# Optimization experiments

Hardware: AMD Instinct MI355X
Metric: run time of the kernel (lower is better)

The kernel has to match this reference:

```python
import jax, jax.numpy as jnp
import numpy as np

N = 400000  # active sparse points (voxels)
K = 27      # 3^3 kernel offsets (dimension=3, kernel_size=3)
C = 32      # inplanes == planes
EPS = 1e-5


def sparse_conv(x, nbr, mask, W, b):
    # gather-GEMM-scatter: for each kernel offset k, out += x[nbr[:,k]] @ W[k]
    # missing neighbors are masked out (MinkowskiEngine skips absent pairs).
    xg = x[nbr] * mask[..., None].astype(x.dtype)   # [N, K, C]
    return jnp.einsum('nkc,kcd->nd', xg, W) + b     # [N, C]


def batchnorm(h, gamma, beta):
    # MinkowskiBatchNorm: per-channel stats over all active points
    mean = jnp.mean(h, axis=0)
    var = jnp.mean(jnp.square(h - mean), axis=0)
    return (h - mean) * jax.lax.rsqrt(var + EPS) * gamma + beta


def setup_inputs() -> dict:
    key = jax.random.key(0)
    ks = jax.random.split(key, 13)
    x = jax.random.normal(ks[0], (N, C), dtype=jnp.float32)
    nbr1 = jax.random.randint(ks[1], (N, K), 0, N, dtype=jnp.int32)
    mask1 = jax.random.randint(ks[2], (N, K), 0, 2, dtype=jnp.int32).astype(bool)
    nbr2 = jax.random.randint(ks[3], (N, K), 0, N, dtype=jnp.int32)
    mask2 = jax.random.randint(ks[4], (N, K), 0, 2, dtype=jnp.int32).astype(bool)
    s = 1.0 / np.sqrt(K * C)  # kaiming-ish scale for sparse conv kernels
    W1 = jax.random.normal(ks[5], (K, C, C), dtype=jnp.float32) * s
    b1 = jax.random.normal(ks[6], (C,), dtype=jnp.float32) * 0.01
    W2 = jax.random.normal(ks[7], (K, C, C), dtype=jnp.float32) * s
    b2 = jax.random.normal(ks[8], (C,), dtype=jnp.float32) * 0.01
    gamma1 = jnp.ones((C,), jnp.float32)
    beta1 = jnp.zeros((C,), jnp.float32)
    gamma2 = jnp.ones((C,), jnp.float32)
    beta2 = jnp.zeros((C,), jnp.float32)
    return dict(x=x, W1=W1, b1=b1, gamma1=gamma1, beta1=beta1,
                W2=W2, b2=b2, gamma2=gamma2, beta2=beta2,
                nbr1=nbr1, mask1=mask1, nbr2=nbr2, mask2=mask2)


def reference(x, W1, b1, gamma1, beta1, W2, b2, gamma2, beta2,
              nbr1, mask1, nbr2, mask2):
    residual = x  # downsample = Identity (stride=1)
    out = sparse_conv(x, nbr1, mask1, W1, b1)
    out = jax.nn.relu(batchnorm(out, gamma1, beta1))
    out = sparse_conv(out, nbr2, mask2, W2, b2)
    out = batchnorm(out, gamma2, beta2)
    out = out + residual  # drop_path=0.0 -> Identity
    return jax.nn.relu(out)
```

## Files before the change

### kernel.cpp

```cpp
#include <hip/hip_runtime.h>

#define NPTS 400000
#define KK 27
#define CC 32
#define EPSV 1e-5f
#define LSTRIDE 29

using bf8_t = __attribute__((ext_vector_type(8))) __bf16;
using f4_t  = __attribute__((ext_vector_type(4))) float;
using us8_t = __attribute__((ext_vector_type(8))) unsigned short;

__device__ __forceinline__ unsigned short f2bf(float f) {
    unsigned int u = __float_as_uint(f);
    u += 0x7FFF + ((u >> 16) & 1u);
    return (unsigned short)(u >> 16);
}

#define WBLOCKS 216
__global__ __launch_bounds__(256) void cvt_all(
    const float* __restrict__ x,
    const float* __restrict__ W1, const float* __restrict__ W2,
    unsigned short* __restrict__ xb,
    unsigned short* __restrict__ Wt1, unsigned short* __restrict__ Wt2,
    float* __restrict__ sums)
{
    const int bid = blockIdx.x;
    if (bid < WBLOCKS) {
        if (bid == 0) sums[threadIdx.x] = 0.f;
        const int id = bid * 256 + threadIdx.x;
        const int which = id >= KK * CC * CC;
        const int t = which ? id - KK * CC * CC : id;
        const int k = t >> 10, d = (t >> 5) & 31, c = t & 31;
        const float* W = which ? W2 : W1;
        unsigned short* Wt = which ? Wt2 : Wt1;
        Wt[t] = f2bf(W[k * 1024 + c * CC + d]);
        return;
    }
    const size_t base = ((size_t)(bid - WBLOCKS) * 256 + threadIdx.x) * 8;
    if (base >= (size_t)NPTS * CC) return;
    const f4_t v0 = __builtin_nontemporal_load((const f4_t*)(x + base));
    const f4_t v1 = __builtin_nontemporal_load((const f4_t*)(x + base + 4));
    us8_t o;
#pragma unroll
    for (int j = 0; j < 8; ++j) o[j] = f2bf(j < 4 ? v0[j] : v1[j - 4]);
    *(us8_t*)(xb + base) = o;
}

__global__ __launch_bounds__(512, 6) void conv_mfma(
    const unsigned short* __restrict__ xb,
    const unsigned short* __restrict__ Wt,
    const float* __restrict__ bias,
    const int* __restrict__ nbr,
    const int* __restrict__ mask,
    float* __restrict__ out,
    float* __restrict__ sums)
{
    __shared__ int lidx[128 * LSTRIDE];
    __shared__ float rs[8][CC], rq[8][CC];

    const int t = threadIdx.x;
    const int P0 = blockIdx.x * 128;

    const int* nb = nbr + (size_t)P0 * KK;
    const int* mb = mask + (size_t)P0 * KK;
    for (int i = t; i < 128 * KK; i += 512) {
        const int p = i / KK;
        const int k = i - p * KK;
        const int nv = __builtin_nontemporal_load(nb + i);
        const int mv = __builtin_nontemporal_load(mb + i);
        lidx[p * LSTRIDE + k] = mv ? nv : -1;
    }
    __syncthreads();

    const int wave = t >> 6;
    const int lane = t & 63;
    const int m = lane & 15;
    const int q = lane >> 4;
    const int p0 = P0 + wave * 16;

    const int* rowA = lidx + (wave * 16 + m) * LSTRIDE;

    f4_t acc00 = {}, acc01 = {};

#pragma unroll
    for (int kb = 0; kb < 3; ++kb) {
        int idx[9];
#pragma unroll
        for (int j = 0; j < 9; ++j) idx[j] = rowA[kb * 9 + j];
        bf8_t A0[9];
#pragma unroll
        for (int j = 0; j < 9; ++j) {
            bf8_t t0 = {};
            if (idx[j] >= 0) t0 = *(const bf8_t*)(xb + (size_t)idx[j] * CC + q * 8);
            A0[j] = t0;
        }
#pragma unroll
        for (int j = 0; j < 9; ++j) {
            const unsigned short* wk = Wt + (kb * 9 + j) * (CC * CC) + q * 8;
            const bf8_t w0 = *(const bf8_t*)(wk + m * CC);
            const bf8_t w1 = *(const bf8_t*)(wk + (m + 16) * CC);
            acc00 = __builtin_amdgcn_mfma_f32_16x16x32_bf16(A0[j], w0, acc00, 0, 0, 0);
            acc01 = __builtin_amdgcn_mfma_f32_16x16x32_bf16(A0[j], w1, acc01, 0, 0, 0);
        }
    }

    const float b0 = bias[m], b1 = bias[m + 16];
    float s0 = 0.f, q0 = 0.f, s1 = 0.f, q1 = 0.f;
    const int prow = p0 + q * 4;
#pragma unroll
    for (int r = 0; r < 4; ++r) {
        const float v0 = acc00[r] + b0;
        const float v1 = acc01[r] + b1;
        __builtin_nontemporal_store(v0, out + (size_t)(prow + r) * CC + m);
        __builtin_nontemporal_store(v1, out + (size_t)(prow + r) * CC + m + 16);
        s0 += v0; q0 += v0 * v0;
        s1 += v1; q1 += v1 * v1;
    }
    s0 += __shfl_down(s0, 32, 64); s0 += __shfl_down(s0, 16, 64);
    q0 += __shfl_down(q0, 32, 64); q0 += __shfl_down(q0, 16, 64);
    s1 += __shfl_down(s1, 32, 64); s1 += __shfl_down(s1, 16, 64);
    q1 += __shfl_down(q1, 32, 64); q1 += __shfl_down(q1, 16, 64);

    if (lane < 16) {
        rs[wave][m] = s0;      rq[wave][m] = q0;
        rs[wave][m + 16] = s1; rq[wave][m + 16] = q1;
    }
    __syncthreads();
    if (t < CC) {
        float ssum = 0.f, qsum = 0.f;
#pragma unroll
        for (int w = 0; w < 8; ++w) { ssum += rs[w][t]; qsum += rq[w][t]; }
        atomicAdd(&sums[t], ssum);
        atomicAdd(&sums[CC + t], qsum);
    }
}

__global__ __launch_bounds__(256) void bn_relu_bf16(
    const float* __restrict__ h, const float* __restrict__ sums,
    const float* __restrict__ gamma, const float* __restrict__ beta,
    unsigned short* __restrict__ buf)
{
    const size_t base = ((size_t)blockIdx.x * 256 + threadIdx.x) * 8;
    if (base >= (size_t)NPTS * CC) return;
    const int d0 = (int)(base & (CC - 1));
    const f4_t v0 = __builtin_nontemporal_load((const f4_t*)(h + base));
    const f4_t v1 = __builtin_nontemporal_load((const f4_t*)(h + base + 4));
    us8_t o;
#pragma unroll
    for (int j = 0; j < 8; ++j) {
        const int d = d0 + j;
        const float mean = sums[d] * (1.f / NPTS);
        const float var = sums[CC + d] * (1.f / NPTS) - mean * mean;
        const float sc = gamma[d] * rsqrtf(var + EPSV);
        const float x = (j < 4 ? v0[j] : v1[j - 4]);
        o[j] = f2bf(fmaxf((x - mean) * sc + beta[d], 0.f));
    }
    *(us8_t*)(buf + base) = o;
}

__global__ __launch_bounds__(256) void bn_res_relu_kernel(
    float* __restrict__ out, const float* __restrict__ sums,
    const float* __restrict__ gamma, const float* __restrict__ beta,
    const float* __restrict__ x)
{
    const size_t i = (size_t)blockIdx.x * 256 + threadIdx.x;
    const size_t base = i * 4;
    if (base >= (size_t)NPTS * CC) return;
    const int d0 = (int)(base & (CC - 1));
    const f4_t v  = __builtin_nontemporal_load((const f4_t*)(out + base));
    const f4_t rx = __builtin_nontemporal_load((const f4_t*)(x + base));
    f4_t r;
#pragma unroll
    for (int j = 0; j < 4; ++j) {
        const int d = d0 + j;
        const float mean = sums[d] * (1.f / NPTS);
        const float var = sums[CC + d] * (1.f / NPTS) - mean * mean;
        const float sc = gamma[d] * rsqrtf(var + EPSV);
        r[j] = fmaxf((v[j] - mean) * sc + beta[d] + rx[j], 0.f);
    }
    __builtin_nontemporal_store(r, (f4_t*)(out + base));
}

extern "C" void kernel_launch(void* const* d_in, const int* in_sizes, int n_in,
                              void* d_out, int out_size, void* d_ws, size_t ws_size,
                              hipStream_t stream) {
    const float* x   = (const float*)d_in[0];
    const float* W1  = (const float*)d_in[1];
    const float* b1  = (const float*)d_in[2];
    const float* g1  = (const float*)d_in[3];
    const float* be1 = (const float*)d_in[4];
    const float* W2  = (const float*)d_in[5];
    const float* b2  = (const float*)d_in[6];
    const float* g2  = (const float*)d_in[7];
    const float* be2 = (const float*)d_in[8];
    const int* nbr1  = (const int*)d_in[9];
    const int* mask1 = (const int*)d_in[10];
    const int* nbr2  = (const int*)d_in[11];
    const int* mask2 = (const int*)d_in[12];

    float* out = (float*)d_out;

    float* sums          = (float*)d_ws;
    unsigned short* xbuf = (unsigned short*)((char*)d_ws + 1024);
    unsigned short* Wt1  = xbuf + (size_t)NPTS * CC;
    unsigned short* Wt2  = Wt1 + KK * CC * CC;

    const int cvt_blocks = WBLOCKS + (NPTS * CC / 8 + 255) / 256;

    cvt_all<<<cvt_blocks, 256, 0, stream>>>(x, W1, W2, xbuf, Wt1, Wt2, sums);
    conv_mfma<<<NPTS / 128, 512, 0, stream>>>(xbuf, Wt1, b1, nbr1, mask1, out, sums);
    bn_relu_bf16<<<(NPTS * CC / 8 + 255) / 256, 256, 0, stream>>>(out, sums, g1, be1, xbuf);
    conv_mfma<<<NPTS / 128, 512, 0, stream>>>(xbuf, Wt2, b2, nbr2, mask2, out, sums + 64);
    bn_res_relu_kernel<<<(NPTS * CC / 4 + 255) / 256, 256, 0, stream>>>(out, sums + 64, g2, be2, x);
}
```

Before: 511.9 us.

## Fuse BN1+ReLU into conv2 gather and store conv outputs as bf16

Removes the standalone BN1+ReLU pass: conv1 now writes bf16 pre-activations into the output buffer, and conv2 applies the per-channel scale/shift and ReLU to each gathered neighbor row before the MFMA. Conv2 also writes bf16 output into the xbuf region, which the final BN+residual+ReLU kernel reads. This removes one full elementwise pass and halves intermediate traffic. In exchange, BN1 math is redone on every gathered row (27 times per point), and the pre-BN values are rounded to bf16 before normalization.

After: 530.2 us. 1.04x slower.

```diff
diff --git a/kernel.cpp b/kernel.cpp
--- a/kernel.cpp
+++ b/kernel.cpp
@@ -14,6 +14,9 @@
     unsigned int u = __float_as_uint(f);
     u += 0x7FFF + ((u >> 16) & 1u);
     return (unsigned short)(u >> 16);
+}
+__device__ __forceinline__ float bf2f(unsigned short s) {
+    return __uint_as_float((unsigned)s << 16);
 }
 
 #define WBLOCKS 216
@@ -46,13 +49,13 @@
     *(us8_t*)(xb + base) = o;
 }
 
-__global__ __launch_bounds__(512, 6) void conv_mfma(
+__global__ __launch_bounds__(512, 6) void conv1_mfma(
     const unsigned short* __restrict__ xb,
     const unsigned short* __restrict__ Wt,
     const float* __restrict__ bias,
     const int* __restrict__ nbr,
     const int* __restrict__ mask,
-    float* __restrict__ out,
+    unsigned short* __restrict__ hb,
     float* __restrict__ sums)
 {
     __shared__ int lidx[128 * LSTRIDE];
@@ -111,8 +114,8 @@
     for (int r = 0; r < 4; ++r) {
         const float v0 = acc00[r] + b0;
         const float v1 = acc01[r] + b1;
-        __builtin_nontemporal_store(v0, out + (size_t)(prow + r) * CC + m);
-        __builtin_nontemporal_store(v1, out + (size_t)(prow + r) * CC + m + 16);
+        __builtin_nontemporal_store(f2bf(v0), hb + (size_t)(prow + r) * CC + m);
+        __builtin_nontemporal_store(f2bf(v1), hb + (size_t)(prow + r) * CC + m + 16);
         s0 += v0; q0 += v0 * v0;
         s1 += v1; q1 += v1 * v1;
     }
@@ -135,50 +138,145 @@
     }
 }
 
-__global__ __launch_bounds__(256) void bn_relu_bf16(
-    const float* __restrict__ h, const float* __restrict__ sums,
+__global__ __launch_bounds__(512, 6) void conv2_mfma(
+    const unsigned short* __restrict__ hb,
+    const unsigned short* __restrict__ Wt,
+    const float* __restrict__ bias,
+    const float* __restrict__ g1, const float* __restrict__ be1,
+    const float* __restrict__ sums1,
+    const int* __restrict__ nbr,
+    const int* __restrict__ mask,
+    unsigned short* __restrict__ h2b,
+    float* __restrict__ sums)
+{
+    __shared__ int lidx[128 * LSTRIDE];
+    __shared__ float rs[8][CC], rq[8][CC];
+
+    const int t = threadIdx.x;
+    const int P0 = blockIdx.x * 128;
+
+    const int* nb = nbr + (size_t)P0 * KK;
+    const int* mb = mask + (size_t)P0 * KK;
+    for (int i = t; i < 128 * KK; i += 512) {
+        const int p = i / KK;
+        const int k = i - p * KK;
+        const int nv = __builtin_nontemporal_load(nb + i);
+        const int mv = __builtin_nontemporal_load(mb + i);
+        lidx[p * LSTRIDE + k] = mv ? nv : -1;
+    }
+    __syncthreads();
+
+    const int wave = t >> 6;
+    const int lane = t & 63;
+    const int m = lane & 15;
+    const int q = lane >> 4;
+    const int p0 = P0 + wave * 16;
+
+    float sc_[8], sh_[8];
+#pragma unroll
+    for (int e = 0; e < 8; ++e) {
+        const int c = q * 8 + e;
+        const float mean = sums1[c] * (1.f / NPTS);
+        const float var = sums1[CC + c] * (1.f / NPTS) - mean * mean;
+        const float s = g1[c] * rsqrtf(var + EPSV);
+        sc_[e] = s;
+        sh_[e] = be1[c] - mean * s;
+    }
+
+    const int* rowA = lidx + (wave * 16 + m) * LSTRIDE;
+
+    f4_t acc00 = {}, acc01 = {};
+
+#pragma unroll
+    for (int kb = 0; kb < 3; ++kb) {
+        int idx[9];
+#pragma unroll
+        for (int j = 0; j < 9; ++j) idx[j] = rowA[kb * 9 + j];
+        bf8_t A0[9];
+#pragma unroll
+        for (int j = 0; j < 9; ++j) {
+            bf8_t a = {};
+            if (idx[j] >= 0) {
+                const us8_t raw = *(const us8_t*)(hb + (size_t)idx[j] * CC + q * 8);
+                us8_t o;
+#pragma unroll
+                for (int e = 0; e < 8; ++e)
+                    o[e] = f2bf(fmaxf(bf2f(raw[e]) * sc_[e] + sh_[e], 0.f));
+                a = __builtin_bit_cast(bf8_t, o);
+            }
+            A0[j] = a;
+        }
+#pragma unroll
+        for (int j = 0; j < 9; ++j) {
+            const unsigned short* wk = Wt + (kb * 9 + j) * (CC * CC) + q * 8;
+            const bf8_t w0 = *(const bf8_t*)(wk + m * CC);
+            const bf8_t w1 = *(const bf8_t*)(wk + (m + 16) * CC);
+            acc00 = __builtin_amdgcn_mfma_f32_16x16x32_bf16(A0[j], w0, acc00, 0, 0, 0);
+            acc01 = __builtin_amdgcn_mfma_f32_16x16x32_bf16(A0[j], w1, acc01, 0, 0, 0);
+        }
+    }
+
+    const float b0 = bias[m], b1 = bias[m + 16];
+    float s0 = 0.f, q0 = 0.f, s1 = 0.f, q1 = 0.f;
+    const int prow = p0 + q * 4;
+#pragma unroll
+    for (int r = 0; r < 4; ++r) {
+        const float v0 = acc00[r] + b0;
+        const float v1 = acc01[r] + b1;
+        __builtin_nontemporal_store(f2bf(v0), h2b + (size_t)(prow + r) * CC + m);
+        __builtin_nontemporal_store(f2bf(v1), h2b + (size_t)(prow + r) * CC + m + 16);
+        s0 += v0; q0 += v0 * v0;
+        s1 += v1; q1 += v1 * v1;
+    }
+    s0 += __shfl_down(s0, 32, 64); s0 += __shfl_down(s0, 16, 64);
+    q0 += __shfl_down(q0, 32, 64); q0 += __shfl_down(q0, 16, 64);
+    s1 += __shfl_down(s1, 32, 64); s1 += __shfl_down(s1, 16, 64);
+    q1 += __shfl_down(q1, 32, 64); q1 += __shfl_down(q1, 16, 64);
+
+    if (lane < 16) {
+        rs[wave][m] = s0;      rq[wave][m] = q0;
+        rs[wave][m + 16] = s1; rq[wave][m + 16] = q1;
+    }
+    __syncthreads();
+    if (t < CC) {
+        float ssum = 0.f, qsum = 0.f;
+#pragma unroll
+        for (int w = 0; w < 8; ++w) { ssum += rs[w][t]; qsum += rq[w][t]; }
+        atomicAdd(&sums[t], ssum);
+        atomicAdd(&sums[CC + t], qsum);
+    }
+}
+
+__global__ __launch_bounds__(256) void bn_res_relu_kernel(
+    const unsigned short* __restrict__ h2b, const float* __restrict__ sums,
     const float* __restrict__ gamma, const float* __restrict__ beta,
-    unsigned short* __restrict__ buf)
+    const float* __restrict__ x, float* __restrict__ out)
 {
     const size_t base = ((size_t)blockIdx.x * 256 + threadIdx.x) * 8;
     if (base >= (size_t)NPTS * CC) return;
     const int d0 = (int)(base & (CC - 1));
-    const f4_t v0 = __builtin_nontemporal_load((const f4_t*)(h + base));
-    const f4_t v1 = __builtin_nontemporal_load((const f4_t*)(h + base + 4));
-    us8_t o;
+    float sc_[8], sh_[8];
 #pragma unroll
     for (int j = 0; j < 8; ++j) {
         const int d = d0 + j;
         const float mean = sums[d] * (1.f / NPTS);
         const float var = sums[CC + d] * (1.f / NPTS) - mean * mean;
-        const float sc = gamma[d] * rsqrtf(var + EPSV);
-        const float x = (j < 4 ? v0[j] : v1[j - 4]);
-        o[j] = f2bf(fmaxf((x - mean) * sc + beta[d], 0.f));
-    }
-    *(us8_t*)(buf + base) = o;
-}
-
-__global__ __launch_bounds__(256) void bn_res_relu_kernel(
-    float* __restrict__ out, const float* __restrict__ sums,
-    const float* __restrict__ gamma, const float* __restrict__ beta,
-    const float* __restrict__ x)
-{
-    const size_t i = (size_t)blockIdx.x * 256 + threadIdx.x;
-    const size_t base = i * 4;
-    if (base >= (size_t)NPTS * CC) return;
-    const int d0 = (int)(base & (CC - 1));
-    const f4_t v  = __builtin_nontemporal_load((const f4_t*)(out + base));
-    const f4_t rx = __builtin_nontemporal_load((const f4_t*)(x + base));
-    f4_t r;
-#pragma unroll
-    for (int j = 0; j < 4; ++j) {
-        const int d = d0 + j;
-        const float mean = sums[d] * (1.f / NPTS);
-        const float var = sums[CC + d] * (1.f / NPTS) - mean * mean;
-        const float sc = gamma[d] * rsqrtf(var + EPSV);
-        r[j] = fmaxf((v[j] - mean) * sc + beta[d] + rx[j], 0.f);
-    }
-    __builtin_nontemporal_store(r, (f4_t*)(out + base));
+        const float s = gamma[d] * rsqrtf(var + EPSV);
+        sc_[j] = s;
+        sh_[j] = beta[d] - mean * s;
+    }
+    const us8_t hv = __builtin_nontemporal_load((const us8_t*)(h2b + base));
+    const f4_t x0 = __builtin_nontemporal_load((const f4_t*)(x + base));
+    const f4_t x1 = __builtin_nontemporal_load((const f4_t*)(x + base + 4));
+    f4_t r0, r1;
+#pragma unroll
+    for (int j = 0; j < 8; ++j) {
+        const float xv = (j < 4 ? x0[j] : x1[j - 4]);
+        const float v = fmaxf(bf2f(hv[j]) * sc_[j] + sh_[j] + xv, 0.f);
+        if (j < 4) r0[j] = v; else r1[j - 4] = v;
+    }
+    __builtin_nontemporal_store(r0, (f4_t*)(out + base));
+    __builtin_nontemporal_store(r1, (f4_t*)(out + base + 4));
 }
 
 extern "C" void kernel_launch(void* const* d_in, const int* in_sizes, int n_in,
@@ -204,12 +302,15 @@
     unsigned short* xbuf = (unsigned short*)((char*)d_ws + 1024);
     unsigned short* Wt1  = xbuf + (size_t)NPTS * CC;
     unsigned short* Wt2  = Wt1 + KK * CC * CC;
+    unsigned short* h1b  = (unsigned short*)out;
+    unsigned short* h2b  = xbuf;
 
     const int cvt_blocks = WBLOCKS + (NPTS * CC / 8 + 255) / 256;
 
     cvt_all<<<cvt_blocks, 256, 0, stream>>>(x, W1, W2, xbuf, Wt1, Wt2, sums);
-    conv_mfma<<<NPTS / 128, 512, 0, stream>>>(xbuf, Wt1, b1, nbr1, mask1, out, sums);
-    bn_relu_bf16<<<(NPTS * CC / 8 + 255) / 256, 256, 0, stream>>>(out, sums, g1, be1, xbuf);
-    conv_mfma<<<NPTS / 128, 512, 0, stream>>>(xbuf, Wt2, b2, nbr2, mask2, out, sums + 64);
-    bn_res_relu_kernel<<<(NPTS * CC / 4 + 255) / 256, 256, 0, stream>>>(out, sums + 64, g2, be2, x);
-}
+    conv1_mfma<<<NPTS / 128, 512, 0, stream>>>(xbuf, Wt1, b1, nbr1, mask1, h1b, sums);
+    conv2_mfma<<<NPTS / 128, 512, 0, stream>>>(h1b, Wt2, b2, g1, be1, sums,
+                                               nbr2, mask2, h2b, sums + 64);
+    bn_res_relu_kernel<<<(NPTS * CC / 8 + 255) / 256, 256, 0, stream>>>(
+        h2b, sums + 64, g2, be2, x, out);
+}
```
